# Performance work log

Measured on AMD Instinct MI355X. Metric: run time of the kernel, lower is better.

Reference implementation:

```python
import jax, jax.numpy as jnp
import numpy as np

N = 50000
E = 800000
IN_DIM = 256
HID = 64
HEADS = 4
OUT_DIM = 32
NEG_SLOPE = 0.2


def gat_conv(x, edge_index, W, a_src, a_dst, bias, heads, out_ch, concat):
    """PyG-style GATConv (eval mode, add_self_loops=True).
    x: [N, F_in]; edge_index: [2, E'] with row0=src, row1=dst.
    W: [F_in, heads*out_ch]; a_src/a_dst: [heads, out_ch]; bias: [heads*out_ch] or [out_ch].
    """
    n = x.shape[0]
    # add self loops
    loops = jnp.arange(n, dtype=edge_index.dtype)
    src = jnp.concatenate([edge_index[0], loops])
    dst = jnp.concatenate([edge_index[1], loops])

    h = (x @ W).reshape(n, heads, out_ch)              # [N, H, C]
    alpha_s = jnp.einsum('nhc,hc->nh', h, a_src)       # [N, H]
    alpha_d = jnp.einsum('nhc,hc->nh', h, a_dst)       # [N, H]
    e = alpha_s[src] + alpha_d[dst]                    # [E', H]
    e = jnp.where(e >= 0, e, NEG_SLOPE * e)            # leaky_relu

    # segment softmax over incoming edges of each dst node
    m = jax.ops.segment_max(e, dst, num_segments=n)    # [N, H]
    ex = jnp.exp(e - m[dst])
    denom = jax.ops.segment_sum(ex, dst, num_segments=n)
    alpha = ex / (denom[dst] + 1e-16)                  # [E', H]

    msg = h[src] * alpha[:, :, None]                   # [E', H, C]
    out = jax.ops.segment_sum(msg, dst, num_segments=n)  # [N, H, C]
    out = out.reshape(n, heads * out_ch) if concat else out.mean(axis=1)
    return out + bias


def setup_inputs() -> dict:
    key = jax.random.key(0)
    ks = jax.random.split(key, 10)
    x = jax.random.normal(ks[0], (N, IN_DIM), dtype=jnp.float32)
    edge_index = jax.random.randint(ks[1], (2, E), 0, N, dtype=jnp.int32)
    s1 = 1.0 / np.sqrt(IN_DIM)
    s2 = 1.0 / np.sqrt(HEADS * HID)
    return {
        'x': x,
        'edge_index': edge_index,
        'W1': jax.random.normal(ks[2], (IN_DIM, HEADS * HID), dtype=jnp.float32) * s1,
        'a_src1': jax.random.normal(ks[3], (HEADS, HID), dtype=jnp.float32) * s2,
        'a_dst1': jax.random.normal(ks[4], (HEADS, HID), dtype=jnp.float32) * s2,
        'b1': jnp.zeros((HEADS * HID,), dtype=jnp.float32),
        'W2': jax.random.normal(ks[5], (HEADS * HID, OUT_DIM), dtype=jnp.float32) * s2,
        'a_src2': jax.random.normal(ks[6], (1, OUT_DIM), dtype=jnp.float32) * 0.125,
        'a_dst2': jax.random.normal(ks[7], (1, OUT_DIM), dtype=jnp.float32) * 0.125,
        'b2': jnp.zeros((OUT_DIM,), dtype=jnp.float32),
    }


def reference(x, edge_index, W1, a_src1, a_dst1, b1, W2, a_src2, a_dst2, b2):
    h = gat_conv(x, edge_index, W1, a_src1, a_dst1, b1, HEADS, HID, concat=True)
    h = jax.nn.elu(h)
    out = gat_conv(h, edge_index, W2, a_src2, a_dst2, b2, 1, OUT_DIM, concat=False)
    return out
```

## Files before the change

### kernel.cpp

```cpp
#include <hip/hip_runtime.h>

#define NEG_SLOPE 0.2f
#define CAP 64
#define CSTRIDE 16
#define LOG2E 1.44269504f

typedef short bf16x8 __attribute__((ext_vector_type(8)));
typedef float f32x4 __attribute__((ext_vector_type(4)));
typedef _Float16 half2v __attribute__((ext_vector_type(2)));
typedef _Float16 half4v __attribute__((ext_vector_type(4)));
typedef _Float16 half8v __attribute__((ext_vector_type(8)));

__device__ inline short bf16_rne(float x) {
    unsigned u = __float_as_uint(x);
    unsigned r = u + 0x7FFFu + ((u >> 16) & 1u);
    return (short)(r >> 16);
}

__device__ inline float fast_exp2(float x) {
#if __has_builtin(__builtin_amdgcn_exp2f)
    return __builtin_amdgcn_exp2f(x);
#else
    return exp2f(x);
#endif
}


__global__ void k_prepw(const float* __restrict__ W1, short* __restrict__ Wt,
                        const float* __restrict__ W2, _Float16* __restrict__ W2t,
                        int* __restrict__ cursor, int* __restrict__ col, int N) {
    int colc = blockIdx.x;
    int k = threadIdx.x;
    Wt[(size_t)colc * 256 + k] = bf16_rne(W1[(size_t)k * 256 + colc]);
    if (colc < 32) W2t[(size_t)colc * 256 + k] = (_Float16)W2[(size_t)k * 32 + colc];
    int gid = blockIdx.x * 256 + threadIdx.x;
    if (gid < N) {
        cursor[(size_t)gid * CSTRIDE] = 1;
        col[(size_t)gid * CAP] = gid;
    }
}


__global__ void k_scatter(const int* __restrict__ src, const int* __restrict__ dst,
                          int* cursor, int* col, int E) {
    int i = blockIdx.x * 256 + threadIdx.x;
    if (i < E) {
        int d = dst[i];
        int p = atomicAdd(&cursor[(size_t)d * CSTRIDE], 1);
        if (p < CAP) col[(size_t)d * CAP + p] = src[i];
    }
}


__global__ __launch_bounds__(256) void k_gemm1(
        const float* __restrict__ x, const short* __restrict__ Wt,
        const float* __restrict__ a_src, const float* __restrict__ a_dst,
        _Float16* __restrict__ h1, float* __restrict__ as1, float* __restrict__ ad1, int N) {
    __shared__ short Ab[64 * 40];
    __shared__ short Bb[256 * 40];
    const int tid = threadIdx.x;
    const int lane = tid & 63;
    const int wc = tid >> 6;
    const int row0 = blockIdx.x * 64;
    const int m15 = lane & 15, quad = lane >> 4;

    f32x4 acc[4][4] = {};

    const int arow = tid >> 2;
    const int akseg = (tid & 3) * 8;

    for (int k0 = 0; k0 < 256; k0 += 32) {
        {
            int row = row0 + arow;
            float vals[8];
            if (row < N) {
                float4 v0 = *(const float4*)(x + (size_t)row * 256 + k0 + akseg);
                float4 v1 = *(const float4*)(x + (size_t)row * 256 + k0 + akseg + 4);
                vals[0] = v0.x; vals[1] = v0.y; vals[2] = v0.z; vals[3] = v0.w;
                vals[4] = v1.x; vals[5] = v1.y; vals[6] = v1.z; vals[7] = v1.w;
            } else {
#pragma unroll
                for (int i = 0; i < 8; ++i) vals[i] = 0.f;
            }
            short buf[8];
#pragma unroll
            for (int i = 0; i < 8; ++i) buf[i] = bf16_rne(vals[i]);
            *(bf16x8*)&Ab[arow * 40 + akseg] = *(bf16x8*)&buf[0];
        }
        {
#pragma unroll
            for (int s = 0; s < 4; ++s)
                *(bf16x8*)&Bb[tid * 40 + s * 8] =
                    *(const bf16x8*)(Wt + (size_t)tid * 256 + k0 + s * 8);
        }
        __syncthreads();
        bf16x8 ab[4];
#pragma unroll
        for (int mt = 0; mt < 4; ++mt)
            ab[mt] = *(const bf16x8*)&Ab[(mt * 16 + m15) * 40 + quad * 8];
#pragma unroll
        for (int nt = 0; nt < 4; ++nt) {
            int nn = wc * 64 + nt * 16 + m15;
            bf16x8 bb = *(const bf16x8*)&Bb[nn * 40 + quad * 8];
#pragma unroll
            for (int mt = 0; mt < 4; ++mt)
                acc[mt][nt] = __builtin_amdgcn_mfma_f32_16x16x32_bf16(ab[mt], bb, acc[mt][nt], 0, 0, 0);
        }
        __syncthreads();
    }
    const int head = wc;
#pragma unroll
    for (int mt = 0; mt < 4; ++mt) {
        float va[4] = {0.f, 0.f, 0.f, 0.f};
        float vd[4] = {0.f, 0.f, 0.f, 0.f};
#pragma unroll
        for (int nt = 0; nt < 4; ++nt) {
            int colg = wc * 64 + nt * 16 + m15;
            float asv = a_src[colg];
            float adv = a_dst[colg];
#pragma unroll
            for (int r = 0; r < 4; ++r) {
                float accv = acc[mt][nt][r];
                int row = row0 + mt * 16 + quad * 4 + r;
                if (row < N) h1[(size_t)row * 256 + colg] = (_Float16)accv;
                va[r] = fmaf(accv, asv, va[r]);
                vd[r] = fmaf(accv, adv, vd[r]);
            }
        }
#pragma unroll
        for (int r = 0; r < 4; ++r) {
#pragma unroll
            for (int mq = 1; mq < 16; mq <<= 1) {
                va[r] += __shfl_xor(va[r], mq);
                vd[r] += __shfl_xor(vd[r], mq);
            }
            int row = row0 + mt * 16 + quad * 4 + r;
            if (m15 == 0 && row < N) {
                as1[(size_t)row * 4 + head] = va[r] * LOG2E;
                ad1[(size_t)row * 4 + head] = vd[r] * LOG2E;
            }
        }
    }
}


__global__ __launch_bounds__(256) void k_fuse1(
        const _Float16* __restrict__ h1, const float* __restrict__ as1,
        const float* __restrict__ ad1, const int* __restrict__ cursor,
        const int* __restrict__ col, const float* __restrict__ b1,
        const _Float16* __restrict__ W2t, const float* __restrict__ a_s2,
        const float* __restrict__ a_d2, _Float16* __restrict__ z,
        float* __restrict__ as2, float* __restrict__ ad2, int N) {
    __shared__ _Float16 W2s[32 * 264];
    __shared__ _Float16 h2s[4 * 256];
    const int tid = threadIdx.x;
    const int l = tid & 63;
    const int wave = tid >> 6;
    const int n = blockIdx.x * 4 + wave;

    for (int i8 = tid; i8 < 1024; i8 += 256) {
        int elem = i8 * 8;
        int row = elem >> 8, k = elem & 255;
        *(half8v*)&W2s[row * 264 + k] = *(const half8v*)(W2t + (size_t)row * 256 + k);
    }
    __syncthreads();
    if (n >= N) return;

    const int head = l >> 4;
    const int beg = n * CAP;
    int deg = __builtin_amdgcn_readfirstlane(cursor[(size_t)n * CSTRIDE]);
    if (deg > CAP) deg = CAP;
    int colv = 0;
    if (l < deg) colv = col[beg + l];
    float adv = ad1[(size_t)n * 4 + head];

    f32x4 a0 = {}, a1 = {}, a2 = {}, a3 = {};
    float s0 = 0.f, s1 = 0.f, s2 = 0.f, s3 = 0.f;
    int j = 0;
    for (; j + 3 < deg; j += 4) {
        int c0 = __builtin_amdgcn_readlane(colv, j);
        int c1 = __builtin_amdgcn_readlane(colv, j + 1);
        int c2 = __builtin_amdgcn_readlane(colv, j + 2);
        int c3 = __builtin_amdgcn_readlane(colv, j + 3);
        float e0 = as1[(size_t)c0 * 4 + head] + adv;
        float e1 = as1[(size_t)c1 * 4 + head] + adv;
        float e2 = as1[(size_t)c2 * 4 + head] + adv;
        float e3 = as1[(size_t)c3 * 4 + head] + adv;
        e0 = fmaxf(e0, NEG_SLOPE * e0); e1 = fmaxf(e1, NEG_SLOPE * e1);
        e2 = fmaxf(e2, NEG_SLOPE * e2); e3 = fmaxf(e3, NEG_SLOPE * e3);
        float p0 = fast_exp2(e0), p1 = fast_exp2(e1);
        float p2 = fast_exp2(e2), p3 = fast_exp2(e3);
        half4v h0 = *((const half4v*)(h1 + (size_t)c0 * 256) + l);
        half4v hv1 = *((const half4v*)(h1 + (size_t)c1 * 256) + l);
        half4v h2 = *((const half4v*)(h1 + (size_t)c2 * 256) + l);
        half4v h3 = *((const half4v*)(h1 + (size_t)c3 * 256) + l);
        s0 += p0; s1 += p1; s2 += p2; s3 += p3;
        a0 += __builtin_convertvector(h0, f32x4) * p0;
        a1 += __builtin_convertvector(hv1, f32x4) * p1;
        a2 += __builtin_convertvector(h2, f32x4) * p2;
        a3 += __builtin_convertvector(h3, f32x4) * p3;
    }
    for (; j < deg; ++j) {
        int c0 = __builtin_amdgcn_readlane(colv, j);
        float e0 = as1[(size_t)c0 * 4 + head] + adv;
        e0 = fmaxf(e0, NEG_SLOPE * e0);
        float p0 = fast_exp2(e0);
        half4v h0 = *((const half4v*)(h1 + (size_t)c0 * 256) + l);
        s0 += p0;
        a0 += __builtin_convertvector(h0, f32x4) * p0;
    }
    f32x4 at = (a0 + a1) + (a2 + a3);
    float iv = 1.f / ((s0 + s1) + (s2 + s3) + 1e-16f);
    float4 bb = *(const float4*)(b1 + l * 4);
    float4 v;
    v.x = at[0] * iv + bb.x;
    v.y = at[1] * iv + bb.y;
    v.z = at[2] * iv + bb.z;
    v.w = at[3] * iv + bb.w;
    v.x = (v.x > 0.f) ? v.x : (__expf(v.x) - 1.f);
    v.y = (v.y > 0.f) ? v.y : (__expf(v.y) - 1.f);
    v.z = (v.z > 0.f) ? v.z : (__expf(v.z) - 1.f);
    v.w = (v.w > 0.f) ? v.w : (__expf(v.w) - 1.f);
    half4v hv;
    hv.x = (_Float16)v.x; hv.y = (_Float16)v.y; hv.z = (_Float16)v.z; hv.w = (_Float16)v.w;
    *((half4v*)(h2s + wave * 256) + l) = hv;

    int c = l & 31;
    int kh = (l >> 5) * 128;
    const _Float16* hrow = h2s + wave * 256 + kh;
    const _Float16* wrow = W2s + c * 264 + kh;
    float accz = 0.f;
#pragma unroll
    for (int k = 0; k < 128; k += 8) {
        half8v hz = *(const half8v*)(hrow + k);
        half8v wz = *(const half8v*)(wrow + k);
#if __has_builtin(__builtin_amdgcn_fdot2)
        accz = __builtin_amdgcn_fdot2(__builtin_shufflevector(hz, hz, 0, 1),
                                      __builtin_shufflevector(wz, wz, 0, 1), accz, false);
        accz = __builtin_amdgcn_fdot2(__builtin_shufflevector(hz, hz, 2, 3),
                                      __builtin_shufflevector(wz, wz, 2, 3), accz, false);
        accz = __builtin_amdgcn_fdot2(__builtin_shufflevector(hz, hz, 4, 5),
                                      __builtin_shufflevector(wz, wz, 4, 5), accz, false);
        accz = __builtin_amdgcn_fdot2(__builtin_shufflevector(hz, hz, 6, 7),
                                      __builtin_shufflevector(wz, wz, 6, 7), accz, false);
#else
        accz = fmaf((float)hz[0], (float)wz[0], accz);
        accz = fmaf((float)hz[1], (float)wz[1], accz);
        accz = fmaf((float)hz[2], (float)wz[2], accz);
        accz = fmaf((float)hz[3], (float)wz[3], accz);
        accz = fmaf((float)hz[4], (float)wz[4], accz);
        accz = fmaf((float)hz[5], (float)wz[5], accz);
        accz = fmaf((float)hz[6], (float)wz[6], accz);
        accz = fmaf((float)hz[7], (float)wz[7], accz);
#endif
    }
    accz += __shfl_xor(accz, 32);
    float za = accz * a_s2[c];
    float zd = accz * a_d2[c];
#pragma unroll
    for (int mq = 1; mq < 32; mq <<= 1) {
        za += __shfl_xor(za, mq);
        zd += __shfl_xor(zd, mq);
    }
    if (l < 32) z[(size_t)n * 32 + c] = (_Float16)accz;
    if (l == 0) {
        as2[n] = za * LOG2E;
        ad2[n] = zd * LOG2E;
    }
}


__global__ void k_gather2(const _Float16* __restrict__ z, const float* __restrict__ as2,
                          const float* __restrict__ ad2, const int* __restrict__ cursor,
                          const int* __restrict__ col, const float* __restrict__ b2,
                          float* __restrict__ out, int N) {
    int n = blockIdx.x * 4 + (threadIdx.x >> 6);
    if (n >= N) return;
    int l = threadIdx.x & 63;
    int eo = l >> 3;
    int cg = l & 7;
    int beg = n * CAP;
    int deg = __builtin_amdgcn_readfirstlane(cursor[(size_t)n * CSTRIDE]);
    if (deg > CAP) deg = CAP;
    int colv = 0;
    if (l < deg) colv = col[beg + l];
    float adn = ad2[n];
    f32x4 acc = {};
    float s = 0.f;

    const int nst = (deg + 7) >> 3;
    int srcA = __shfl(colv, eo);
    float aA = as2[srcA];
    half4v zA = *((const half4v*)(z + (size_t)srcA * 32) + cg);
    for (int t = 0; t < nst; ++t) {
        int srcB = 0; float aB = 0.f; half4v zB = {};
        if (t + 1 < nst) {
            srcB = __shfl(colv, (t + 1) * 8 + eo);
            aB = as2[srcB];
            zB = *((const half4v*)(z + (size_t)srcB * 32) + cg);
        }
        float e = aA + adn;
        e = fmaxf(e, NEG_SLOPE * e);
        float p = (t * 8 + eo < deg) ? fast_exp2(e) : 0.f;
        s += p;
        acc += __builtin_convertvector(zA, f32x4) * p;
        srcA = srcB; aA = aB; zA = zB;
    }
    float ax = acc[0], ay = acc[1], az = acc[2], aw = acc[3];
#pragma unroll
    for (int mq = 8; mq < 64; mq <<= 1) {
        ax += __shfl_xor(ax, mq);
        ay += __shfl_xor(ay, mq);
        az += __shfl_xor(az, mq);
        aw += __shfl_xor(aw, mq);
        s += __shfl_xor(s, mq);
    }
    if (eo == 0) {
        float iv = 1.f / (s + 1e-16f);
        float4 bb = *(const float4*)(b2 + cg * 4);
        float4 v;
        v.x = ax * iv + bb.x;
        v.y = ay * iv + bb.y;
        v.z = az * iv + bb.z;
        v.w = aw * iv + bb.w;
        *(float4*)(out + (size_t)n * 32 + cg * 4) = v;
    }
}


extern "C" void kernel_launch(void* const* d_in, const int* in_sizes, int n_in,
                              void* d_out, int out_size, void* d_ws, size_t ws_size,
                              hipStream_t stream) {
    const float* x    = (const float*)d_in[0];
    const int*   ei   = (const int*)d_in[1];
    const float* W1   = (const float*)d_in[2];
    const float* a_s1 = (const float*)d_in[3];
    const float* a_d1 = (const float*)d_in[4];
    const float* b1   = (const float*)d_in[5];
    const float* W2   = (const float*)d_in[6];
    const float* a_s2 = (const float*)d_in[7];
    const float* a_d2 = (const float*)d_in[8];
    const float* b2   = (const float*)d_in[9];
    float* out = (float*)d_out;

    const int N = in_sizes[0] / 256;
    const int E = in_sizes[1] / 2;
    const int* srcIdx = ei;
    const int* dstIdx = ei + E;

    char* ws = (char*)d_ws;
    size_t off = 0;
    auto alloc = [&](size_t bytes) {
        void* p = ws + off;
        off += (bytes + 255) & ~(size_t)255;
        return p;
    };
    _Float16* h1   = (_Float16*)alloc((size_t)N * 256 * 2);
    _Float16* z    = (_Float16*)alloc((size_t)N * 32 * 2);
    float* as1    = (float*)alloc((size_t)N * 16);
    float* ad1    = (float*)alloc((size_t)N * 16);
    float* as2    = (float*)alloc((size_t)N * 4);
    float* ad2    = (float*)alloc((size_t)N * 4);
    short* Wt     = (short*)alloc((size_t)256 * 256 * 2);
    _Float16* W2t = (_Float16*)alloc((size_t)32 * 256 * 2);
    int*   cursor = (int*)alloc((size_t)N * CSTRIDE * 4);
    int*   col    = (int*)alloc((size_t)N * CAP * 4);

    k_prepw<<<256, 256, 0, stream>>>(W1, Wt, W2, W2t, cursor, col, N);
    k_scatter<<<(E + 255) / 256, 256, 0, stream>>>(srcIdx, dstIdx, cursor, col, E);

    k_gemm1<<<(N + 63) / 64, 256, 0, stream>>>(x, Wt, a_s1, a_d1, h1, as1, ad1, N);

    k_fuse1<<<(N + 3) / 4, 256, 0, stream>>>(h1, as1, ad1, cursor, col, b1, W2t,
                                             a_s2, a_d2, z, as2, ad2, N);

    k_gather2<<<(N + 3) / 4, 256, 0, stream>>>(z, as2, ad2, cursor, col, b2, out, N);
}
```

Before: 266.6 us.

## Compute attention logits per edge-chunk in parallel and pack cursor array

Result: no change. 263.8 us (-1.1%).

```diff
diff --git a/kernel.cpp b/kernel.cpp
--- a/kernel.cpp
+++ b/kernel.cpp
@@ -2,12 +2,10 @@
 
 #define NEG_SLOPE 0.2f
 #define CAP 64
-#define CSTRIDE 16
 #define LOG2E 1.44269504f
 
 typedef short bf16x8 __attribute__((ext_vector_type(8)));
 typedef float f32x4 __attribute__((ext_vector_type(4)));
-typedef _Float16 half2v __attribute__((ext_vector_type(2)));
 typedef _Float16 half4v __attribute__((ext_vector_type(4)));
 typedef _Float16 half8v __attribute__((ext_vector_type(8)));
 
@@ -35,7 +33,7 @@
     if (colc < 32) W2t[(size_t)colc * 256 + k] = (_Float16)W2[(size_t)k * 32 + colc];
     int gid = blockIdx.x * 256 + threadIdx.x;
     if (gid < N) {
-        cursor[(size_t)gid * CSTRIDE] = 1;
+        cursor[gid] = 1;
         col[(size_t)gid * CAP] = gid;
     }
 }
@@ -46,7 +44,7 @@
     int i = blockIdx.x * 256 + threadIdx.x;
     if (i < E) {
         int d = dst[i];
-        int p = atomicAdd(&cursor[(size_t)d * CSTRIDE], 1);
+        int p = atomicAdd(&cursor[d], 1);
         if (p < CAP) col[(size_t)d * CAP + p] = src[i];
     }
 }
@@ -167,50 +165,65 @@
     if (n >= N) return;
 
     const int head = l >> 4;
+    const int h4 = l & 3;
+    const int slot = l >> 2;
     const int beg = n * CAP;
-    int deg = __builtin_amdgcn_readfirstlane(cursor[(size_t)n * CSTRIDE]);
+    int deg = __builtin_amdgcn_readfirstlane(cursor[n]);
     if (deg > CAP) deg = CAP;
     int colv = 0;
     if (l < deg) colv = col[beg + l];
-    float adv = ad1[(size_t)n * 4 + head];
+    float adv4 = ad1[(size_t)n * 4 + h4];
 
     f32x4 a0 = {}, a1 = {}, a2 = {}, a3 = {};
-    float s0 = 0.f, s1 = 0.f, s2 = 0.f, s3 = 0.f;
-    int j = 0;
-    for (; j + 3 < deg; j += 4) {
-        int c0 = __builtin_amdgcn_readlane(colv, j);
-        int c1 = __builtin_amdgcn_readlane(colv, j + 1);
-        int c2 = __builtin_amdgcn_readlane(colv, j + 2);
-        int c3 = __builtin_amdgcn_readlane(colv, j + 3);
-        float e0 = as1[(size_t)c0 * 4 + head] + adv;
-        float e1 = as1[(size_t)c1 * 4 + head] + adv;
-        float e2 = as1[(size_t)c2 * 4 + head] + adv;
-        float e3 = as1[(size_t)c3 * 4 + head] + adv;
-        e0 = fmaxf(e0, NEG_SLOPE * e0); e1 = fmaxf(e1, NEG_SLOPE * e1);
-        e2 = fmaxf(e2, NEG_SLOPE * e2); e3 = fmaxf(e3, NEG_SLOPE * e3);
-        float p0 = fast_exp2(e0), p1 = fast_exp2(e1);
-        float p2 = fast_exp2(e2), p3 = fast_exp2(e3);
-        half4v h0 = *((const half4v*)(h1 + (size_t)c0 * 256) + l);
-        half4v hv1 = *((const half4v*)(h1 + (size_t)c1 * 256) + l);
-        half4v h2 = *((const half4v*)(h1 + (size_t)c2 * 256) + l);
-        half4v h3 = *((const half4v*)(h1 + (size_t)c3 * 256) + l);
-        s0 += p0; s1 += p1; s2 += p2; s3 += p3;
-        a0 += __builtin_convertvector(h0, f32x4) * p0;
-        a1 += __builtin_convertvector(hv1, f32x4) * p1;
-        a2 += __builtin_convertvector(h2, f32x4) * p2;
-        a3 += __builtin_convertvector(h3, f32x4) * p3;
-    }
-    for (; j < deg; ++j) {
-        int c0 = __builtin_amdgcn_readlane(colv, j);
-        float e0 = as1[(size_t)c0 * 4 + head] + adv;
-        e0 = fmaxf(e0, NEG_SLOPE * e0);
-        float p0 = fast_exp2(e0);
-        half4v h0 = *((const half4v*)(h1 + (size_t)c0 * 256) + l);
-        s0 += p0;
-        a0 += __builtin_convertvector(h0, f32x4) * p0;
-    }
+    float s_all = 0.f;
+
+    const int nck = (deg + 15) >> 4;
+    for (int ck = 0; ck < nck; ++ck) {
+        int idx = ck * 16 + slot;
+        int cidx = __shfl(colv, idx);
+        float av = as1[(size_t)cidx * 4 + h4];
+        float e = av + adv4;
+        e = fmaxf(e, NEG_SLOPE * e);
+        float p = (idx < deg) ? fast_exp2(e) : 0.f;
+        float sc = p;
+        sc += __shfl_xor(sc, 4);
+        sc += __shfl_xor(sc, 8);
+        sc += __shfl_xor(sc, 16);
+        sc += __shfl_xor(sc, 32);
+        s_all += sc;
+
+        int ecnt = deg - ck * 16;
+        if (ecnt > 16) ecnt = 16;
+        int j = 0;
+        for (; j + 3 < ecnt; j += 4) {
+            int c0 = __builtin_amdgcn_readlane(colv, ck * 16 + j + 0);
+            int c1 = __builtin_amdgcn_readlane(colv, ck * 16 + j + 1);
+            int c2 = __builtin_amdgcn_readlane(colv, ck * 16 + j + 2);
+            int c3 = __builtin_amdgcn_readlane(colv, ck * 16 + j + 3);
+            float p0 = __shfl(p, (j + 0) * 4 + head);
+            float p1 = __shfl(p, (j + 1) * 4 + head);
+            float p2 = __shfl(p, (j + 2) * 4 + head);
+            float p3 = __shfl(p, (j + 3) * 4 + head);
+            half4v h0 = *((const half4v*)(h1 + (size_t)c0 * 256) + l);
+            half4v hv1 = *((const half4v*)(h1 + (size_t)c1 * 256) + l);
+            half4v h2 = *((const half4v*)(h1 + (size_t)c2 * 256) + l);
+            half4v h3 = *((const half4v*)(h1 + (size_t)c3 * 256) + l);
+            a0 += __builtin_convertvector(h0, f32x4) * p0;
+            a1 += __builtin_convertvector(hv1, f32x4) * p1;
+            a2 += __builtin_convertvector(h2, f32x4) * p2;
+            a3 += __builtin_convertvector(h3, f32x4) * p3;
+        }
+        for (; j < ecnt; ++j) {
+            int c0 = __builtin_amdgcn_readlane(colv, ck * 16 + j);
+            float p0 = __shfl(p, j * 4 + head);
+            half4v h0 = *((const half4v*)(h1 + (size_t)c0 * 256) + l);
+            a0 += __builtin_convertvector(h0, f32x4) * p0;
+        }
+    }
+
     f32x4 at = (a0 + a1) + (a2 + a3);
-    float iv = 1.f / ((s0 + s1) + (s2 + s3) + 1e-16f);
+    float s = __shfl(s_all, head);
+    float iv = 1.f / (s + 1e-16f);
     float4 bb = *(const float4*)(b1 + l * 4);
     float4 v;
     v.x = at[0] * iv + bb.x;
@@ -280,31 +293,34 @@
     int eo = l >> 3;
     int cg = l & 7;
     int beg = n * CAP;
-    int deg = __builtin_amdgcn_readfirstlane(cursor[(size_t)n * CSTRIDE]);
+    int deg = __builtin_amdgcn_readfirstlane(cursor[n]);
     if (deg > CAP) deg = CAP;
     int colv = 0;
-    if (l < deg) colv = col[beg + l];
+    float azv = 0.f;
+    if (l < deg) {
+        colv = col[beg + l];
+        azv = as2[colv];
+    }
     float adn = ad2[n];
     f32x4 acc = {};
     float s = 0.f;
 
     const int nst = (deg + 7) >> 3;
     int srcA = __shfl(colv, eo);
-    float aA = as2[srcA];
     half4v zA = *((const half4v*)(z + (size_t)srcA * 32) + cg);
     for (int t = 0; t < nst; ++t) {
-        int srcB = 0; float aB = 0.f; half4v zB = {};
+        int srcB = 0; half4v zB = {};
         if (t + 1 < nst) {
             srcB = __shfl(colv, (t + 1) * 8 + eo);
-            aB = as2[srcB];
             zB = *((const half4v*)(z + (size_t)srcB * 32) + cg);
         }
+        float aA = __shfl(azv, t * 8 + eo);
         float e = aA + adn;
         e = fmaxf(e, NEG_SLOPE * e);
         float p = (t * 8 + eo < deg) ? fast_exp2(e) : 0.f;
         s += p;
         acc += __builtin_convertvector(zA, f32x4) * p;
-        srcA = srcB; aA = aB; zA = zB;
+        srcA = srcB; zA = zB;
     }
     float ax = acc[0], ay = acc[1], az = acc[2], aw = acc[3];
 #pragma unroll
@@ -363,7 +379,7 @@
     float* ad2    = (float*)alloc((size_t)N * 4);
     short* Wt     = (short*)alloc((size_t)256 * 256 * 2);
     _Float16* W2t = (_Float16*)alloc((size_t)32 * 256 * 2);
-    int*   cursor = (int*)alloc((size_t)N * CSTRIDE * 4);
+    int*   cursor = (int*)alloc((size_t)N * 4);
     int*   col    = (int*)alloc((size_t)N * CAP * 4);
 
     k_prepw<<<256, 256, 0, stream>>>(W1, Wt, W2, W2t, cursor, col, N);
```
